# Kernel optimization log

Hardware: AMD Instinct MI355X
Metric: run time of the kernel (lower is better)

The kernel has to match this reference:

```python
import jax, jax.numpy as jnp
import numpy as np

B, T, CIN, CH, NBLOCKS, NCLS = 8, 16384, 1, 32, 6, 2


def conv1d(x, w, b, dilation=1):
    # x: [B, T, Cin], w: [K, Cin, Cout] (Keras/WIO layout), 'same' padding
    y = jax.lax.conv_general_dilated(
        x, w, window_strides=(1,), padding='SAME',
        rhs_dilation=(dilation,), dimension_numbers=('NWC', 'WIO', 'NWC'))
    return y + b


def setup_inputs() -> dict:
    key = jax.random.key(0)
    ks = jax.random.split(key, 8)
    s = 0.1  # weight scale
    return {
        'x': jax.random.normal(ks[0], (B, T, CIN), jnp.float32),
        'w_init': jax.random.normal(ks[1], (1, CIN, CH), jnp.float32) * s,
        'b_init': jnp.zeros((CH,), jnp.float32),
        'w_tanh': jax.random.normal(ks[2], (NBLOCKS, 3, CH, CH), jnp.float32) * s,
        'b_tanh': jnp.zeros((NBLOCKS, CH), jnp.float32),
        'w_sig': jax.random.normal(ks[3], (NBLOCKS, 3, CH, CH), jnp.float32) * s,
        'b_sig': jnp.zeros((NBLOCKS, CH), jnp.float32),
        'w_skip': jax.random.normal(ks[4], (NBLOCKS, 1, CH, CH), jnp.float32) * s,
        'b_skip': jnp.zeros((NBLOCKS, CH), jnp.float32),
        'w_final': jax.random.normal(ks[5], (1, CH, CH), jnp.float32) * s,
        'b_final': jnp.zeros((CH,), jnp.float32),
        'w_dense': jax.random.normal(ks[6], (T * CH, NCLS), jnp.float32) * 0.01,
        'b_dense': jnp.zeros((NCLS,), jnp.float32),
    }


def reference(x, w_init, b_init, w_tanh, b_tanh, w_sig, b_sig,
              w_skip, b_skip, w_final, b_final, w_dense, b_dense):
    h = jax.nn.relu(conv1d(x, w_init, b_init))  # [B, T, CH]
    skip_sum = jnp.zeros_like(h)
    for i in range(NBLOCKS):
        d = 2 ** i
        t = jnp.tanh(conv1d(h, w_tanh[i], b_tanh[i], d))
        g = jax.nn.sigmoid(conv1d(h, w_sig[i], b_sig[i], d))
        skip = jax.nn.relu(conv1d(t * g, w_skip[i], b_skip[i]))
        h = skip + h
        skip_sum = skip_sum + skip
    y = jax.nn.relu(skip_sum)
    y = jax.nn.relu(conv1d(y, w_final, b_final))
    y = y.reshape(B, T * CH)
    logits = y @ w_dense + b_dense
    return jax.nn.softmax(logits, axis=-1)
```

## Files before the change

### kernel.cpp

```cpp
#include <hip/hip_runtime.h>
#include <math.h>

#define T_LEN   16384
#define NBATCH  8
#define NBLK    6
#define TILE    256
#define HALO    63
#define NTHR    768
#define NWAVE   12
#define NROWS   384
#define NTILES  64
#define HS      18
#define HBUF    (NROWS * HS)

#define WS_CONV 0
#define WS_SKIP 18432
#define WS_FIN  21504
#define WS_LOG  22016
#define WS_CNT  22032
#define PREP_N  22016
#define PREP_TOT 22036

#define STG_CONV 0
#define STG_SKIP 3072
#define STG_TOT  3584

typedef _Float16 half8 __attribute__((ext_vector_type(8)));
typedef __fp16  fp16x2 __attribute__((ext_vector_type(2)));
typedef float f32x4  __attribute__((ext_vector_type(4)));

union HPK { unsigned u; _Float16 h[2]; fp16x2 pk; };
union AFR { uint2 u2[2]; half8 v; };

__device__ __forceinline__ unsigned packh(float a, float b) {
    HPK r; r.pk = __builtin_amdgcn_cvt_pkrtz(a, b); return r.u;
}
__device__ __forceinline__ float f16a(unsigned p) { HPK r; r.u = p; return (float)r.h[0]; }
__device__ __forceinline__ float f16b(unsigned p) { HPK r; r.u = p; return (float)r.h[1]; }

__device__ __forceinline__ float gated(float a, float b) {
    float ea  = __expf(-2.0f * fabsf(a));
    float fb  = __expf(-b);
    float num = 1.0f - ea;
    float den = (1.0f + ea) * (1.0f + fb);
    float t   = num * __builtin_amdgcn_rcpf(den);
    return __builtin_copysignf(t, a);
}
__device__ __forceinline__ float relu(float x) { return fmaxf(x, 0.0f); }

__device__ __forceinline__ void gl_lds16(const unsigned* g, unsigned* l) {
    __builtin_amdgcn_global_load_lds(
        (const __attribute__((address_space(1))) void*)g,
        (__attribute__((address_space(3))) void*)l, 16, 0, 0);
}

#define MFMA(a, b, c) __builtin_amdgcn_mfma_f32_16x16x32_f16((a), (b), (c), 0, 0, 0)

__global__ void wavenet_prep(const float* __restrict__ wt, const float* __restrict__ wsg,
                             const float* __restrict__ wsk, const float* __restrict__ wfin,
                             unsigned* __restrict__ out)
{
    int id = blockIdx.x * 256 + threadIdx.x;
    if (id >= PREP_TOT) return;
    if (id >= PREP_N) { out[id] = 0u; return; }
    int dw = id & 3, lane = (id >> 2) & 63;
    int g = lane >> 4, nlo = lane & 15;
    int k0 = g * 8 + dw * 2, k1 = k0 + 1;
    float v0, v1;
    if (id < WS_SKIP) {
        int nt = (id >> 8) & 3; int q = id >> 10;
        int tap = q % 3, i = q / 3;
        int chan = 2 * nlo + (nt & 1);
        const float* src = (nt < 2) ? wt : wsg;
        v0 = src[((i * 3 + tap) * 32 + k0) * 32 + chan];
        v1 = src[((i * 3 + tap) * 32 + k1) * 32 + chan];
    } else if (id < WS_FIN) {
        int t = id - WS_SKIP;
        int nt = (t >> 8) & 1; int i = t >> 9;
        int chan = 2 * nlo + nt;
        v0 = wsk[(i * 32 + k0) * 32 + chan];
        v1 = wsk[(i * 32 + k1) * 32 + chan];
    } else {
        int t = id - WS_FIN;
        int nt = (t >> 8) & 1;
        int chan = 2 * nlo + nt;
        v0 = wfin[k0 * 32 + chan];
        v1 = wfin[k1 * 32 + chan];
    }
    HPK r; r.h[0] = (_Float16)v0; r.h[1] = (_Float16)v1;
    out[id] = r.u;
}

__global__ __launch_bounds__(NTHR, 6)
void wavenet_main(const float* __restrict__ x,
                  const float* __restrict__ w_init, const float* __restrict__ b_init,
                  const float* __restrict__ b_tanh, const float* __restrict__ b_sig,
                  const float* __restrict__ b_skip, const float* __restrict__ b_final,
                  const float* __restrict__ b_dense,
                  const float* __restrict__ w_dense,
                  const unsigned* __restrict__ wsB,
                  float* __restrict__ logits, unsigned* __restrict__ counter,
                  float* __restrict__ out)
{
    __shared__ unsigned h_pack[2 * HBUF];
    __shared__ unsigned wstage[STG_TOT];
    __shared__ float x_s[NROWS];
    __shared__ float bias_s[3 * NBLK * 32];
    __shared__ float wib_s[64];
    __shared__ float red[NWAVE][2];

    const int tid  = threadIdx.x;
    const int lane = tid & 63;
    const int wv   = tid >> 6;
    const int tile = blockIdx.x & (NTILES - 1);
    const int b    = blockIdx.x >> 6;
    const int col0 = lane & 15;
    const int g4   = lane >> 4;

    #define STAGE_ITER(it) do {                                                   \
        const unsigned* _s = wsB + (it) * 3072 + wv * 256 + (lane << 2);          \
        gl_lds16(_s, wstage + wv * 256 + (lane << 2));                            \
        if (wv < 2) {                                                             \
            const unsigned* _s2 = wsB + WS_SKIP + (it) * 512 + wv * 256 + (lane << 2); \
            gl_lds16(_s2, wstage + STG_SKIP + wv * 256 + (lane << 2));            \
        }                                                                         \
    } while (0)

    STAGE_ITER(0);

    if (tid < 3 * NBLK * 32) {
        int which = tid / (NBLK * 32), r = tid % (NBLK * 32);
        float v = (which == 0) ? b_tanh[r] : (which == 1) ? b_sig[r] : b_skip[r];
        bias_s[tid] = v;
    } else if (tid < 3 * NBLK * 32 + 64) {
        int r = tid - 3 * NBLK * 32;
        wib_s[r] = (r < 32) ? w_init[r] : b_init[r - 32];
    }

    {
        int j    = tid >> 1;
        int half = tid & 1;
        int tg = tile * TILE - HALO + j;
        bool valid = (tg >= 0) && (tg < T_LEN);
        float xv = valid ? x[(size_t)b * T_LEN + tg] : 0.0f;
        x_s[j] = xv;
        unsigned* hp = &h_pack[j * HS + half * 8];
        #pragma unroll
        for (int q = 0; q < 4; ++q) {
            int ch = (half * 8 + 2 * q) * 2;
            float f0 = relu(fmaf(xv, w_init[ch],     b_init[ch]));
            float f1 = relu(fmaf(xv, w_init[ch + 1], b_init[ch + 1]));
            float f2 = relu(fmaf(xv, w_init[ch + 2], b_init[ch + 2]));
            float f3 = relu(fmaf(xv, w_init[ch + 3], b_init[ch + 3]));
            uint2 pk;
            pk.x = valid ? packh(f0, f1) : 0u;
            pk.y = valid ? packh(f2, f3) : 0u;
            *(uint2*)(hp + 2 * q) = pk;
        }
    }
    __syncthreads();

    #pragma unroll
    for (int i = 0; i < NBLK; ++i) {
        const int d = 1 << i;
        const unsigned* cur = &h_pack[(i & 1) * HBUF];
        unsigned*       nxt = &h_pack[((i + 1) & 1) * HBUF];

        #pragma unroll
        for (int m = 0; m < 2; ++m) {
            const int row0 = wv * 32 + 16 * m;

            f32x4 acc[4];
            #pragma unroll
            for (int nt = 0; nt < 4; ++nt) acc[nt] = (f32x4){0.f, 0.f, 0.f, 0.f};

            #pragma unroll
            for (int tap = 0; tap < 3; ++tap) {
                half8 bw[4];
                #pragma unroll
                for (int nt = 0; nt < 4; ++nt)
                    bw[nt] = *(const half8*)(wstage + (tap * 4 + nt) * 256 + (lane << 2));
                int r = row0 + (tap - 1) * d + col0;
                r = r < 0 ? 0 : (r > NROWS - 1 ? NROWS - 1 : r);
                const unsigned* hp = cur + r * HS + g4 * 4;
                AFR a; a.u2[0] = *(const uint2*)hp; a.u2[1] = *(const uint2*)(hp + 2);
                #pragma unroll
                for (int nt = 0; nt < 4; ++nt)
                    acc[nt] = MFMA(a.v, bw[nt], acc[nt]);
            }

            unsigned hold[4];
            #pragma unroll
            for (int reg = 0; reg < 4; ++reg)
                hold[reg] = cur[(row0 + 4 * g4 + reg) * HS + col0];
            float2 btv = *(const float2*)&bias_s[0 * NBLK * 32 + i * 32 + 2 * col0];
            float2 bsv = *(const float2*)&bias_s[1 * NBLK * 32 + i * 32 + 2 * col0];
            float2 bkv = *(const float2*)&bias_s[2 * NBLK * 32 + i * 32 + 2 * col0];
            half8 skw[2];
            #pragma unroll
            for (int nt = 0; nt < 2; ++nt)
                skw[nt] = *(const half8*)(wstage + STG_SKIP + nt * 256 + (lane << 2));

            if (m == 1 && i + 1 < NBLK) {
                __syncthreads();
                STAGE_ITER(i + 1);
            }

            #pragma unroll
            for (int reg = 0; reg < 4; ++reg) {
                float z0 = gated(acc[0][reg] + btv.x, acc[2][reg] + bsv.x);
                float z1 = gated(acc[1][reg] + btv.y, acc[3][reg] + bsv.y);
                nxt[(row0 + 4 * g4 + reg) * HS + col0] = packh(z0, z1);
            }
            asm volatile("" ::: "memory");
            const unsigned* za = nxt + (row0 + col0) * HS + g4 * 4;
            AFR az; az.u2[0] = *(const uint2*)za; az.u2[1] = *(const uint2*)(za + 2);
            f32x4 s0 = (f32x4){0.f, 0.f, 0.f, 0.f}, s1 = (f32x4){0.f, 0.f, 0.f, 0.f};
            s0 = MFMA(az.v, skw[0], s0);
            s1 = MFMA(az.v, skw[1], s1);
            #pragma unroll
            for (int reg = 0; reg < 4; ++reg) {
                const int row = row0 + 4 * g4 + reg;
                float sk0 = relu(s0[reg] + bkv.x);
                float sk1 = relu(s1[reg] + bkv.y);
                unsigned ph = hold[reg];
                float h0n = sk0 + f16a(ph);
                float h1n = sk1 + f16b(ph);
                unsigned pk;
                if (i != NBLK - 1) {
                    int tgr = tile * TILE - HALO + row;
                    bool vr = (tgr >= 0) && (tgr < T_LEN);
                    pk = vr ? packh(h0n, h1n) : 0u;
                } else {
                    float2 wiv = *(const float2*)&wib_s[2 * col0];
                    float2 biv = *(const float2*)&wib_s[32 + 2 * col0];
                    float xr  = x_s[row];
                    float hi0 = relu(fmaf(xr, wiv.x, biv.x));
                    float hi1 = relu(fmaf(xr, wiv.y, biv.y));
                    pk = packh(relu(h0n - hi0), relu(h1n - hi1));
                }
                nxt[row * HS + col0] = pk;
            }
        }
        __syncthreads();
    }

    float4 wd[2][4];
    #pragma unroll
    for (int mt = 0; mt < 2; ++mt) {
        #pragma unroll
        for (int reg = 0; reg < 4; ++reg) {
            int row = wv * 32 + 16 * mt + 4 * g4 + reg;
            int tgr = tile * TILE - HALO + row;
            tgr = tgr < 0 ? 0 : (tgr > T_LEN - 1 ? T_LEN - 1 : tgr);
            wd[mt][reg] = *(const float4*)&w_dense[((size_t)tgr * 32 + 2 * col0) * 2];
        }
    }

    const unsigned* ybuf = &h_pack[(NBLK & 1) * HBUF];
    half8 fw[2];
    #pragma unroll
    for (int nt = 0; nt < 2; ++nt)
        fw[nt] = *(const half8*)(wsB + WS_FIN + nt * 256 + lane * 4);
    float2 bfv = *(const float2*)&b_final[2 * col0];
    float pa = 0.0f, pb = 0.0f;

    #pragma unroll
    for (int mt = 0; mt < 2; ++mt) {
        const unsigned* ya = ybuf + (wv * 32 + 16 * mt + col0) * HS + g4 * 4;
        AFR ay; ay.u2[0] = *(const uint2*)ya; ay.u2[1] = *(const uint2*)(ya + 2);
        f32x4 f0 = (f32x4){0.f, 0.f, 0.f, 0.f}, f1 = (f32x4){0.f, 0.f, 0.f, 0.f};
        f0 = MFMA(ay.v, fw[0], f0);
        f1 = MFMA(ay.v, fw[1], f1);
        #pragma unroll
        for (int reg = 0; reg < 4; ++reg) {
            int row = wv * 32 + 16 * mt + 4 * g4 + reg;
            if (row >= HALO && row < HALO + TILE) {
                float v0 = relu(f0[reg] + bfv.x);
                float v1 = relu(f1[reg] + bfv.y);
                float4 wv4 = wd[mt][reg];
                pa = fmaf(v0, wv4.x, pa); pb = fmaf(v0, wv4.y, pb);
                pa = fmaf(v1, wv4.z, pa); pb = fmaf(v1, wv4.w, pb);
            }
        }
    }

    #pragma unroll
    for (int off = 32; off > 0; off >>= 1) {
        pa += __shfl_down(pa, off);
        pb += __shfl_down(pb, off);
    }
    if (lane == 0) { red[wv][0] = pa; red[wv][1] = pb; }
    __syncthreads();
    if (wv == 0) {
        if (lane < 2) {
            float s = 0.0f;
            #pragma unroll
            for (int w = 0; w < NWAVE; ++w) s += red[w][lane];
            atomicAdd(&logits[b * 2 + lane], s);
        }
        __threadfence();
        unsigned arrived = 0u;
        if (lane == 0) arrived = atomicAdd(counter, 1u);
        arrived = __builtin_amdgcn_readfirstlane(arrived);
        if (arrived == (unsigned)(NBATCH * NTILES - 1)) {
            __threadfence();
            float l = 0.0f;
            if (lane < 16)
                l = atomicAdd(&logits[lane], 0.0f) + b_dense[lane & 1];
            float lx = __shfl_xor(l, 1);
            float m  = fmaxf(l, lx);
            float e  = __expf(l - m);
            float ex = __shfl_xor(e, 1);
            float r  = e * __builtin_amdgcn_rcpf(e + ex);
            if (lane < 16) out[lane] = r;
        }
    }
    #undef STAGE_ITER
}

extern "C" void kernel_launch(void* const* d_in, const int* in_sizes, int n_in,
                              void* d_out, int out_size, void* d_ws, size_t ws_size,
                              hipStream_t stream) {
    const float* x       = (const float*)d_in[0];
    const float* w_init  = (const float*)d_in[1];
    const float* b_init  = (const float*)d_in[2];
    const float* w_tanh  = (const float*)d_in[3];
    const float* b_tanh  = (const float*)d_in[4];
    const float* w_sig   = (const float*)d_in[5];
    const float* b_sig   = (const float*)d_in[6];
    const float* w_skip  = (const float*)d_in[7];
    const float* b_skip  = (const float*)d_in[8];
    const float* w_final = (const float*)d_in[9];
    const float* b_final = (const float*)d_in[10];
    const float* w_dense = (const float*)d_in[11];
    const float* b_dense = (const float*)d_in[12];

    unsigned* wsB     = (unsigned*)d_ws;
    float*    logits  = (float*)d_ws + WS_LOG;
    unsigned* counter = (unsigned*)d_ws + WS_CNT;

    wavenet_prep<<<(PREP_TOT + 255) / 256, 256, 0, stream>>>(w_tanh, w_sig, w_skip, w_final, wsB);
    wavenet_main<<<NBATCH * NTILES, NTHR, 0, stream>>>(
        x, w_init, b_init, b_tanh, b_sig, b_skip, b_final, b_dense, w_dense,
        wsB, logits, counter, (float*)d_out);
}
```

Before: 123.0 us.

## Swap MFMA operands and permute channels to keep gated output in registers

The gated residual block now runs transposed MFMAs, with weights as the A operand and activations as B. The input channels are permuted so that the gate output's accumulator layout matches the B-fragment layout of the skip MFMA. This removes the LDS round-trip that used to write the gated z values and read them back. Biases are preloaded into the accumulators, one barrier per block is dropped, and the final and dense stages are adapted to the new layout. The catch is more register pressure from holding both segments' fragments live, plus a more intricate channel permutation in the weight prep.

```diff
diff --git a/kernel.cpp b/kernel.cpp
--- a/kernel.cpp
+++ b/kernel.cpp
@@ -38,6 +38,10 @@
 __device__ __forceinline__ float f16a(unsigned p) { HPK r; r.u = p; return (float)r.h[0]; }
 __device__ __forceinline__ float f16b(unsigned p) { HPK r; r.u = p; return (float)r.h[1]; }
 
+__device__ __forceinline__ int perm_ch(int g, int j) {
+    return j < 4 ? 4 * g + j : 16 + 4 * g + (j - 4);
+}
+
 __device__ __forceinline__ float gated(float a, float b) {
     float ea  = __expf(-2.0f * fabsf(a));
     float fb  = __expf(-b);
@@ -65,27 +69,27 @@
     if (id >= PREP_N) { out[id] = 0u; return; }
     int dw = id & 3, lane = (id >> 2) & 63;
     int g = lane >> 4, nlo = lane & 15;
-    int k0 = g * 8 + dw * 2, k1 = k0 + 1;
+    int ci0 = perm_ch(g, 2 * dw), ci1 = perm_ch(g, 2 * dw + 1);
     float v0, v1;
     if (id < WS_SKIP) {
         int nt = (id >> 8) & 3; int q = id >> 10;
         int tap = q % 3, i = q / 3;
-        int chan = 2 * nlo + (nt & 1);
+        int co = (nt & 1) * 16 + nlo;
         const float* src = (nt < 2) ? wt : wsg;
-        v0 = src[((i * 3 + tap) * 32 + k0) * 32 + chan];
-        v1 = src[((i * 3 + tap) * 32 + k1) * 32 + chan];
+        v0 = src[((i * 3 + tap) * 32 + ci0) * 32 + co];
+        v1 = src[((i * 3 + tap) * 32 + ci1) * 32 + co];
     } else if (id < WS_FIN) {
         int t = id - WS_SKIP;
         int nt = (t >> 8) & 1; int i = t >> 9;
-        int chan = 2 * nlo + nt;
-        v0 = wsk[(i * 32 + k0) * 32 + chan];
-        v1 = wsk[(i * 32 + k1) * 32 + chan];
+        int co = nt * 16 + nlo;
+        v0 = wsk[(i * 32 + ci0) * 32 + co];
+        v1 = wsk[(i * 32 + ci1) * 32 + co];
     } else {
         int t = id - WS_FIN;
         int nt = (t >> 8) & 1;
-        int chan = 2 * nlo + nt;
-        v0 = wfin[k0 * 32 + chan];
-        v1 = wfin[k1 * 32 + chan];
+        int co = nt * 16 + nlo;
+        v0 = wfin[ci0 * 32 + co];
+        v1 = wfin[ci1 * 32 + co];
     }
     HPK r; r.h[0] = (_Float16)v0; r.h[1] = (_Float16)v1;
     out[id] = r.u;
@@ -126,6 +130,82 @@
         }                                                                         \
     } while (0)
 
+    #define FRONT_SEG(ROW0, ZF, HOLD) do {                                        \
+        f32x4 acc0 = *(const f32x4*)&bias_s[0 * NBLK * 32 + i * 32 + 4 * g4];     \
+        f32x4 acc1 = *(const f32x4*)&bias_s[0 * NBLK * 32 + i * 32 + 16 + 4 * g4];\
+        f32x4 acc2 = *(const f32x4*)&bias_s[1 * NBLK * 32 + i * 32 + 4 * g4];     \
+        f32x4 acc3 = *(const f32x4*)&bias_s[1 * NBLK * 32 + i * 32 + 16 + 4 * g4];\
+        _Pragma("unroll")                                                         \
+        for (int tap = 0; tap < 3; ++tap) {                                       \
+            half8 aw0 = *(const half8*)(wstage + (tap * 4 + 0) * 256 + (lane << 2)); \
+            half8 aw1 = *(const half8*)(wstage + (tap * 4 + 1) * 256 + (lane << 2)); \
+            half8 aw2 = *(const half8*)(wstage + (tap * 4 + 2) * 256 + (lane << 2)); \
+            half8 aw3 = *(const half8*)(wstage + (tap * 4 + 3) * 256 + (lane << 2)); \
+            int r = (ROW0) + (tap - 1) * d + col0;                                \
+            r = r < 0 ? 0 : (r > NROWS - 1 ? NROWS - 1 : r);                      \
+            const unsigned* hp = cur + r * HS + g4 * 4;                           \
+            AFR bf; bf.u2[0] = *(const uint2*)hp; bf.u2[1] = *(const uint2*)(hp + 2); \
+            acc0 = MFMA(aw0, bf.v, acc0);                                         \
+            acc1 = MFMA(aw1, bf.v, acc1);                                         \
+            acc2 = MFMA(aw2, bf.v, acc2);                                         \
+            acc3 = MFMA(aw3, bf.v, acc3);                                         \
+        }                                                                         \
+        const unsigned* hq = cur + ((ROW0) + col0) * HS + g4 * 4;                 \
+        (HOLD)[0] = *(const uint2*)hq; (HOLD)[1] = *(const uint2*)(hq + 2);       \
+        float za0 = gated(acc0[0], acc2[0]);                                      \
+        float za1 = gated(acc0[1], acc2[1]);                                      \
+        float za2 = gated(acc0[2], acc2[2]);                                      \
+        float za3 = gated(acc0[3], acc2[3]);                                      \
+        float zb0 = gated(acc1[0], acc3[0]);                                      \
+        float zb1 = gated(acc1[1], acc3[1]);                                      \
+        float zb2 = gated(acc1[2], acc3[2]);                                      \
+        float zb3 = gated(acc1[3], acc3[3]);                                      \
+        (ZF).u2[0] = make_uint2(packh(za0, za1), packh(za2, za3));                \
+        (ZF).u2[1] = make_uint2(packh(zb0, zb1), packh(zb2, zb3));                \
+    } while (0)
+
+    #define BACK_SEG(ROW0, ZF, HOLD) do {                                         \
+        f32x4 s0 = *(const f32x4*)&bias_s[2 * NBLK * 32 + i * 32 + 4 * g4];       \
+        f32x4 s1 = *(const f32x4*)&bias_s[2 * NBLK * 32 + i * 32 + 16 + 4 * g4];  \
+        s0 = MFMA(skw[0], (ZF).v, s0);                                            \
+        s1 = MFMA(skw[1], (ZF).v, s1);                                            \
+        const int row = (ROW0) + col0;                                            \
+        float na0 = relu(s0[0]) + f16a((HOLD)[0].x);                              \
+        float na1 = relu(s0[1]) + f16b((HOLD)[0].x);                              \
+        float na2 = relu(s0[2]) + f16a((HOLD)[0].y);                              \
+        float na3 = relu(s0[3]) + f16b((HOLD)[0].y);                              \
+        float nb0 = relu(s1[0]) + f16a((HOLD)[1].x);                              \
+        float nb1 = relu(s1[1]) + f16b((HOLD)[1].x);                              \
+        float nb2 = relu(s1[2]) + f16a((HOLD)[1].y);                              \
+        float nb3 = relu(s1[3]) + f16b((HOLD)[1].y);                              \
+        unsigned pk0, pk1, pk2, pk3;                                              \
+        if (!ilast) {                                                             \
+            int tgr = tile * TILE - HALO + row;                                   \
+            bool vr = (tgr >= 0) && (tgr < T_LEN);                                \
+            pk0 = vr ? packh(na0, na1) : 0u;                                      \
+            pk1 = vr ? packh(na2, na3) : 0u;                                      \
+            pk2 = vr ? packh(nb0, nb1) : 0u;                                      \
+            pk3 = vr ? packh(nb2, nb3) : 0u;                                      \
+        } else {                                                                  \
+            float xr = x_s[row];                                                  \
+            float4 wa = *(const float4*)&wib_s[4 * g4];                           \
+            float4 wb = *(const float4*)&wib_s[16 + 4 * g4];                      \
+            float4 ba = *(const float4*)&wib_s[32 + 4 * g4];                      \
+            float4 bb = *(const float4*)&wib_s[48 + 4 * g4];                      \
+            pk0 = packh(relu(na0 - relu(fmaf(xr, wa.x, ba.x))),                   \
+                        relu(na1 - relu(fmaf(xr, wa.y, ba.y))));                  \
+            pk1 = packh(relu(na2 - relu(fmaf(xr, wa.z, ba.z))),                   \
+                        relu(na3 - relu(fmaf(xr, wa.w, ba.w))));                  \
+            pk2 = packh(relu(nb0 - relu(fmaf(xr, wb.x, bb.x))),                   \
+                        relu(nb1 - relu(fmaf(xr, wb.y, bb.y))));                  \
+            pk3 = packh(relu(nb2 - relu(fmaf(xr, wb.z, bb.z))),                   \
+                        relu(nb3 - relu(fmaf(xr, wb.w, bb.w))));                  \
+        }                                                                         \
+        unsigned* hw = nxt + row * HS + g4 * 4;                                   \
+        *(uint2*)hw = make_uint2(pk0, pk1);                                       \
+        *(uint2*)(hw + 2) = make_uint2(pk2, pk3);                                 \
+    } while (0)
+
     STAGE_ITER(0);
 
     if (tid < 3 * NBLK * 32) {
@@ -147,15 +227,18 @@
         unsigned* hp = &h_pack[j * HS + half * 8];
         #pragma unroll
         for (int q = 0; q < 4; ++q) {
-            int ch = (half * 8 + 2 * q) * 2;
-            float f0 = relu(fmaf(xv, w_init[ch],     b_init[ch]));
-            float f1 = relu(fmaf(xv, w_init[ch + 1], b_init[ch + 1]));
-            float f2 = relu(fmaf(xv, w_init[ch + 2], b_init[ch + 2]));
-            float f3 = relu(fmaf(xv, w_init[ch + 3], b_init[ch + 3]));
-            uint2 pk;
-            pk.x = valid ? packh(f0, f1) : 0u;
-            pk.y = valid ? packh(f2, f3) : 0u;
-            *(uint2*)(hp + 2 * q) = pk;
+            unsigned pk[2];
+            #pragma unroll
+            for (int e = 0; e < 2; ++e) {
+                int D  = half * 8 + 2 * q + e;
+                int s0 = 2 * D, s1 = 2 * D + 1;
+                int c0 = perm_ch(s0 >> 3, s0 & 7);
+                int c1 = perm_ch(s1 >> 3, s1 & 7);
+                float f0 = relu(fmaf(xv, w_init[c0], b_init[c0]));
+                float f1 = relu(fmaf(xv, w_init[c1], b_init[c1]));
+                pk[e] = valid ? packh(f0, f1) : 0u;
+            }
+            *(uint2*)(hp + 2 * q) = make_uint2(pk[0], pk[1]);
         }
     }
     __syncthreads();
@@ -165,123 +248,68 @@
         const int d = 1 << i;
         const unsigned* cur = &h_pack[(i & 1) * HBUF];
         unsigned*       nxt = &h_pack[((i + 1) & 1) * HBUF];
-
-        #pragma unroll
-        for (int m = 0; m < 2; ++m) {
-            const int row0 = wv * 32 + 16 * m;
-
-            f32x4 acc[4];
-            #pragma unroll
-            for (int nt = 0; nt < 4; ++nt) acc[nt] = (f32x4){0.f, 0.f, 0.f, 0.f};
-
-            #pragma unroll
-            for (int tap = 0; tap < 3; ++tap) {
-                half8 bw[4];
-                #pragma unroll
-                for (int nt = 0; nt < 4; ++nt)
-                    bw[nt] = *(const half8*)(wstage + (tap * 4 + nt) * 256 + (lane << 2));
-                int r = row0 + (tap - 1) * d + col0;
-                r = r < 0 ? 0 : (r > NROWS - 1 ? NROWS - 1 : r);
-                const unsigned* hp = cur + r * HS + g4 * 4;
-                AFR a; a.u2[0] = *(const uint2*)hp; a.u2[1] = *(const uint2*)(hp + 2);
-                #pragma unroll
-                for (int nt = 0; nt < 4; ++nt)
-                    acc[nt] = MFMA(a.v, bw[nt], acc[nt]);
-            }
-
-            unsigned hold[4];
-            #pragma unroll
-            for (int reg = 0; reg < 4; ++reg)
-                hold[reg] = cur[(row0 + 4 * g4 + reg) * HS + col0];
-            float2 btv = *(const float2*)&bias_s[0 * NBLK * 32 + i * 32 + 2 * col0];
-            float2 bsv = *(const float2*)&bias_s[1 * NBLK * 32 + i * 32 + 2 * col0];
-            float2 bkv = *(const float2*)&bias_s[2 * NBLK * 32 + i * 32 + 2 * col0];
-            half8 skw[2];
-            #pragma unroll
-            for (int nt = 0; nt < 2; ++nt)
-                skw[nt] = *(const half8*)(wstage + STG_SKIP + nt * 256 + (lane << 2));
-
-            if (m == 1 && i + 1 < NBLK) {
-                __syncthreads();
-                STAGE_ITER(i + 1);
-            }
-
-            #pragma unroll
-            for (int reg = 0; reg < 4; ++reg) {
-                float z0 = gated(acc[0][reg] + btv.x, acc[2][reg] + bsv.x);
-                float z1 = gated(acc[1][reg] + btv.y, acc[3][reg] + bsv.y);
-                nxt[(row0 + 4 * g4 + reg) * HS + col0] = packh(z0, z1);
-            }
-            asm volatile("" ::: "memory");
-            const unsigned* za = nxt + (row0 + col0) * HS + g4 * 4;
-            AFR az; az.u2[0] = *(const uint2*)za; az.u2[1] = *(const uint2*)(za + 2);
-            f32x4 s0 = (f32x4){0.f, 0.f, 0.f, 0.f}, s1 = (f32x4){0.f, 0.f, 0.f, 0.f};
-            s0 = MFMA(az.v, skw[0], s0);
-            s1 = MFMA(az.v, skw[1], s1);
-            #pragma unroll
-            for (int reg = 0; reg < 4; ++reg) {
-                const int row = row0 + 4 * g4 + reg;
-                float sk0 = relu(s0[reg] + bkv.x);
-                float sk1 = relu(s1[reg] + bkv.y);
-                unsigned ph = hold[reg];
-                float h0n = sk0 + f16a(ph);
-                float h1n = sk1 + f16b(ph);
-                unsigned pk;
-                if (i != NBLK - 1) {
-                    int tgr = tile * TILE - HALO + row;
-                    bool vr = (tgr >= 0) && (tgr < T_LEN);
-                    pk = vr ? packh(h0n, h1n) : 0u;
-                } else {
-                    float2 wiv = *(const float2*)&wib_s[2 * col0];
-                    float2 biv = *(const float2*)&wib_s[32 + 2 * col0];
-                    float xr  = x_s[row];
-                    float hi0 = relu(fmaf(xr, wiv.x, biv.x));
-                    float hi1 = relu(fmaf(xr, wiv.y, biv.y));
-                    pk = packh(relu(h0n - hi0), relu(h1n - hi1));
-                }
-                nxt[row * HS + col0] = pk;
-            }
-        }
-        __syncthreads();
-    }
-
-    float4 wd[2][4];
+        const bool ilast = (i == NBLK - 1);
+
+        half8 skw[2];
+        skw[0] = *(const half8*)(wstage + STG_SKIP + (lane << 2));
+        skw[1] = *(const half8*)(wstage + STG_SKIP + 256 + (lane << 2));
+
+        AFR zf0, zf1; uint2 hold0[2], hold1[2];
+        FRONT_SEG(wv * 32,      zf0, hold0);
+        FRONT_SEG(wv * 32 + 16, zf1, hold1);
+
+        if (!ilast) {
+            __syncthreads();
+            STAGE_ITER(i + 1);
+        }
+
+        BACK_SEG(wv * 32,      zf0, hold0);
+        BACK_SEG(wv * 32 + 16, zf1, hold1);
+
+        if (!ilast) __syncthreads();
+    }
+    asm volatile("" ::: "memory");
+
+    float4 wdp[2][4];
     #pragma unroll
     for (int mt = 0; mt < 2; ++mt) {
-        #pragma unroll
-        for (int reg = 0; reg < 4; ++reg) {
-            int row = wv * 32 + 16 * mt + 4 * g4 + reg;
-            int tgr = tile * TILE - HALO + row;
-            tgr = tgr < 0 ? 0 : (tgr > T_LEN - 1 ? T_LEN - 1 : tgr);
-            wd[mt][reg] = *(const float4*)&w_dense[((size_t)tgr * 32 + 2 * col0) * 2];
-        }
+        int row = wv * 32 + mt * 16 + col0;
+        int tgr = tile * TILE - HALO + row;
+        tgr = tgr < 0 ? 0 : (tgr > T_LEN - 1 ? T_LEN - 1 : tgr);
+        const float* base = w_dense + (size_t)tgr * 64;
+        wdp[mt][0] = *(const float4*)(base + 8 * g4);
+        wdp[mt][1] = *(const float4*)(base + 8 * g4 + 4);
+        wdp[mt][2] = *(const float4*)(base + 32 + 8 * g4);
+        wdp[mt][3] = *(const float4*)(base + 32 + 8 * g4 + 4);
     }
 
     const unsigned* ybuf = &h_pack[(NBLK & 1) * HBUF];
-    half8 fw[2];
-    #pragma unroll
-    for (int nt = 0; nt < 2; ++nt)
-        fw[nt] = *(const half8*)(wsB + WS_FIN + nt * 256 + lane * 4);
-    float2 bfv = *(const float2*)&b_final[2 * col0];
+    half8 fwA[2];
+    fwA[0] = *(const half8*)(wsB + WS_FIN + (lane << 2));
+    fwA[1] = *(const half8*)(wsB + WS_FIN + 256 + (lane << 2));
+    float4 bfa = *(const float4*)&b_final[4 * g4];
+    float4 bfb = *(const float4*)&b_final[16 + 4 * g4];
     float pa = 0.0f, pb = 0.0f;
 
     #pragma unroll
     for (int mt = 0; mt < 2; ++mt) {
-        const unsigned* ya = ybuf + (wv * 32 + 16 * mt + col0) * HS + g4 * 4;
+        const int row = wv * 32 + mt * 16 + col0;
+        const unsigned* ya = ybuf + row * HS + g4 * 4;
         AFR ay; ay.u2[0] = *(const uint2*)ya; ay.u2[1] = *(const uint2*)(ya + 2);
-        f32x4 f0 = (f32x4){0.f, 0.f, 0.f, 0.f}, f1 = (f32x4){0.f, 0.f, 0.f, 0.f};
-        f0 = MFMA(ay.v, fw[0], f0);
-        f1 = MFMA(ay.v, fw[1], f1);
-        #pragma unroll
-        for (int reg = 0; reg < 4; ++reg) {
-            int row = wv * 32 + 16 * mt + 4 * g4 + reg;
-            if (row >= HALO && row < HALO + TILE) {
-                float v0 = relu(f0[reg] + bfv.x);
-                float v1 = relu(f1[reg] + bfv.y);
-                float4 wv4 = wd[mt][reg];
-                pa = fmaf(v0, wv4.x, pa); pb = fmaf(v0, wv4.y, pb);
-                pa = fmaf(v1, wv4.z, pa); pb = fmaf(v1, wv4.w, pb);
-            }
+        f32x4 f0 = (f32x4){bfa.x, bfa.y, bfa.z, bfa.w};
+        f32x4 f1 = (f32x4){bfb.x, bfb.y, bfb.z, bfb.w};
+        f0 = MFMA(fwA[0], ay.v, f0);
+        f1 = MFMA(fwA[1], ay.v, f1);
+        if (row >= HALO && row < HALO + TILE) {
+            float v;
+            v = relu(f0[0]); pa = fmaf(v, wdp[mt][0].x, pa); pb = fmaf(v, wdp[mt][0].y, pb);
+            v = relu(f0[1]); pa = fmaf(v, wdp[mt][0].z, pa); pb = fmaf(v, wdp[mt][0].w, pb);
+            v = relu(f0[2]); pa = fmaf(v, wdp[mt][1].x, pa); pb = fmaf(v, wdp[mt][1].y, pb);
+            v = relu(f0[3]); pa = fmaf(v, wdp[mt][1].z, pa); pb = fmaf(v, wdp[mt][1].w, pb);
+            v = relu(f1[0]); pa = fmaf(v, wdp[mt][2].x, pa); pb = fmaf(v, wdp[mt][2].y, pb);
+            v = relu(f1[1]); pa = fmaf(v, wdp[mt][2].z, pa); pb = fmaf(v, wdp[mt][2].w, pb);
+            v = relu(f1[2]); pa = fmaf(v, wdp[mt][3].x, pa); pb = fmaf(v, wdp[mt][3].y, pb);
+            v = relu(f1[3]); pa = fmaf(v, wdp[mt][3].z, pa); pb = fmaf(v, wdp[mt][3].w, pb);
         }
     }
 
@@ -317,6 +345,8 @@
         }
     }
     #undef STAGE_ITER
+    #undef FRONT_SEG
+    #undef BACK_SEG
 }
 
 extern "C" void kernel_launch(void* const* d_in, const int* in_sizes, int n_in,
```

After: 134.8 us. 1.1x slower.
